# Optimization experiments

Measured on AMD Instinct MI355X. Metric: run time of the kernel, lower is better.

Reference implementation:

```python
import jax, jax.numpy as jnp
import numpy as np

DIM = 768
HEADS = 12
HEAD_DIM = DIM // HEADS
HIDDEN = 4 * DIM
LS_INIT = 1e-5
EPS = 1e-5


def layernorm(x, g, b):
    mu = jnp.mean(x, axis=-1, keepdims=True)
    var = jnp.mean(jnp.square(x - mu), axis=-1, keepdims=True)
    return (x - mu) * jax.lax.rsqrt(var + EPS) * g + b


def setup_inputs() -> dict:
    key = jax.random.key(0)
    ks = jax.random.split(key, 8)
    s = lambda fan_in: 1.0 / np.sqrt(fan_in)
    return {
        "x": jax.random.normal(ks[0], (8, 1024, DIM), dtype=jnp.float32),
        "ln1_g": jnp.ones((DIM,), jnp.float32),
        "ln1_b": jnp.zeros((DIM,), jnp.float32),
        "w_qkv": jax.random.uniform(ks[1], (3 * DIM, DIM), jnp.float32, -s(DIM), s(DIM)),
        "w_proj": jax.random.uniform(ks[2], (DIM, DIM), jnp.float32, -s(DIM), s(DIM)),
        "b_proj": jnp.zeros((DIM,), jnp.float32),
        "ls1_g": jnp.full((DIM,), LS_INIT, jnp.float32),
        "ln2_g": jnp.ones((DIM,), jnp.float32),
        "ln2_b": jnp.zeros((DIM,), jnp.float32),
        "w_fc1": jax.random.uniform(ks[3], (HIDDEN, DIM), jnp.float32, -s(DIM), s(DIM)),
        "b_fc1": jnp.zeros((HIDDEN,), jnp.float32),
        "w_fc2": jax.random.uniform(ks[4], (DIM, HIDDEN), jnp.float32, -s(HIDDEN), s(HIDDEN)),
        "b_fc2": jnp.zeros((DIM,), jnp.float32),
        "ls2_g": jnp.full((DIM,), LS_INIT, jnp.float32),
    }


def reference(x, ln1_g, ln1_b, w_qkv, w_proj, b_proj, ls1_g,
              ln2_g, ln2_b, w_fc1, b_fc1, w_fc2, b_fc2, ls2_g):
    B, N, C = x.shape
    # --- attention branch ---
    h = layernorm(x, ln1_g, ln1_b)
    qkv = h @ w_qkv.T  # [B,N,3C]
    qkv = qkv.reshape(B, N, 3, HEADS, HEAD_DIM)
    q, k, v = qkv[:, :, 0], qkv[:, :, 1], qkv[:, :, 2]  # [B,N,H,D]
    scale = 1.0 / np.sqrt(HEAD_DIM)
    attn = jnp.einsum("bqhd,bkhd->bhqk", q, k) * scale
    attn = jax.nn.softmax(attn, axis=-1)
    o = jnp.einsum("bhqk,bkhd->bqhd", attn, v).reshape(B, N, C)
    o = o @ w_proj.T + b_proj
    x = x + ls1_g * o
    # --- MLP branch ---
    h = layernorm(x, ln2_g, ln2_b)
    h = jax.nn.gelu(h @ w_fc1.T + b_fc1, approximate=False)
    h = h @ w_fc2.T + b_fc2
    x = x + ls2_g * h
    return x
```

## Files before the change

### kernel.cpp

```cpp
#include <hip/hip_runtime.h>
#include <cstdint>
#include <cstddef>

typedef __bf16 bf16x8 __attribute__((ext_vector_type(8)));
typedef __bf16 bf16x4 __attribute__((ext_vector_type(4)));
typedef float f32x4 __attribute__((ext_vector_type(4)));
typedef int i32x4 __attribute__((ext_vector_type(4)));
typedef int i32x8 __attribute__((ext_vector_type(8)));

__device__ __forceinline__ void gload16(const void* g, void* l) {
  __builtin_amdgcn_global_load_lds((const __attribute__((address_space(1))) void*)g,
                                   (__attribute__((address_space(3))) void*)l, 16, 0, 0);
}

__device__ __forceinline__ float exp2_fast(float x) {
  float r;
  asm("v_exp_f32 %0, %1" : "=v"(r) : "v"(x));
  return r;
}
__device__ __forceinline__ float rcp_fast(float x) {
  float r;
  asm("v_rcp_f32 %0, %1" : "=v"(r) : "v"(x));
  return r;
}

__device__ __forceinline__ unsigned char f32_to_fp8(float x) {
  int p = __builtin_amdgcn_cvt_pk_fp8_f32(x, 0.f, 0, false);
  return (unsigned char)(p & 0xff);
}
__device__ __forceinline__ unsigned int f32x4_to_fp8x4(float a, float b, float c, float d) {
  int p0 = __builtin_amdgcn_cvt_pk_fp8_f32(a, b, 0, false);
  int p1 = __builtin_amdgcn_cvt_pk_fp8_f32(c, d, 0, false);
  return (unsigned int)((p0 & 0xffff) | ((p1 & 0xffff) << 16));
}

template<int N> __device__ __forceinline__ void wait_vm() {
  if constexpr (N == 0) asm volatile("s_waitcnt vmcnt(0)" ::: "memory");
  else if constexpr (N == 4) asm volatile("s_waitcnt vmcnt(4)" ::: "memory");
  else if constexpr (N == 6) asm volatile("s_waitcnt vmcnt(6)" ::: "memory");
}

#define S_BARRIER() __builtin_amdgcn_s_barrier()
#define WAIT_VM4()  asm volatile("s_waitcnt vmcnt(4)" ::: "memory")
#define WAIT_VM0()  asm volatile("s_waitcnt vmcnt(0)" ::: "memory")
#define WAIT_LGKM() asm volatile("s_waitcnt lgkmcnt(0)" ::: "memory")

__global__ __launch_bounds__(256) void ln_kernel(const float* __restrict__ x,
    const float* __restrict__ g, const float* __restrict__ b,
    unsigned char* __restrict__ out)
{
  __shared__ float red[8];
  const int row = blockIdx.x, t = threadIdx.x;
  const float* xr = x + (size_t)row * 768;
  float v0 = xr[t], v1 = xr[t + 256], v2 = xr[t + 512];
  float s = v0 + v1 + v2;
  float q = v0 * v0 + v1 * v1 + v2 * v2;
  #pragma unroll
  for (int off = 32; off > 0; off >>= 1) {
    s += __shfl_xor(s, off, 64);
    q += __shfl_xor(q, off, 64);
  }
  const int w = t >> 6;
  if ((t & 63) == 0) { red[w] = s; red[4 + w] = q; }
  __syncthreads();
  s = red[0] + red[1] + red[2] + red[3];
  q = red[4] + red[5] + red[6] + red[7];
  const float mu = s * (1.0f / 768.0f);
  const float var = q * (1.0f / 768.0f) - mu * mu;
  const float rstd = rsqrtf(var + 1e-5f);
  unsigned char* orow = out + (size_t)row * 768;
  orow[t]       = f32_to_fp8((v0 - mu) * rstd * g[t]       + b[t]);
  orow[t + 256] = f32_to_fp8((v1 - mu) * rstd * g[t + 256] + b[t + 256]);
  orow[t + 512] = f32_to_fp8((v2 - mu) * rstd * g[t + 512] + b[t + 512]);
}

__global__ __launch_bounds__(256) void cast4_kernel(
    const float* __restrict__ i0, const float* __restrict__ i1,
    const float* __restrict__ i2, const float* __restrict__ i3,
    unsigned char* __restrict__ o0, unsigned char* __restrict__ o1,
    unsigned char* __restrict__ o2, unsigned char* __restrict__ o3)
{
  const int n0 = 2304 * 768 / 4, n1 = 768 * 768 / 4;
  const int n2 = 3072 * 768 / 4, n3 = 768 * 3072 / 4;
  const int total = n0 + n1 + n2 + n3;
  for (int i = blockIdx.x * 256 + threadIdx.x; i < total; i += gridDim.x * 256) {
    const float* in; unsigned char* out; int j = i;
    if (j < n0) { in = i0; out = o0; }
    else if ((j -= n0) < n1) { in = i1; out = o1; }
    else if ((j -= n1) < n2) { in = i2; out = o2; }
    else { j -= n2; in = i3; out = o3; }
    float4 v = ((const float4*)in)[j];
    ((unsigned int*)out)[j] = f32x4_to_fp8x4(v.x, v.y, v.z, v.w);
  }
}

template<int MODE>
__global__ __launch_bounds__(256) void gemm_kernel(
    const unsigned char* __restrict__ A, const unsigned char* __restrict__ W, int K,
    const float* __restrict__ bias, const float* __restrict__ resid,
    const float* __restrict__ ls, float* __restrict__ outf,
    unsigned char* __restrict__ outb,
    __bf16* __restrict__ qo, __bf16* __restrict__ ko, __bf16* __restrict__ vo)
{
  constexpr int BM = 128, BN = 64, BK = 128;
  constexpr int FM = 4, FN = 2;
  __shared__ unsigned char As[2 * BM * BK];
  __shared__ unsigned char Bs[2 * BN * BK];

  const int nx = gridDim.x;
  const int nwg = nx * gridDim.y;
  const int orig = blockIdx.x + nx * blockIdx.y;
  const int nid = (orig & 7) * (nwg >> 3) + (orig >> 3);
  const int bx = nid % nx, by = nid / nx;

  const int t = threadIdx.x;
  const int lane = t & 63;
  const int w = t >> 6;
  const int wm = w >> 1, wn = w & 1;
  const int m0 = by * BM, n0 = bx * BN;
  const int rl = lane & 15, gs = lane >> 4;

  f32x4 acc[FM][FN];
  #pragma unroll
  for (int i = 0; i < FM; ++i)
    #pragma unroll
    for (int j = 0; j < FN; ++j) acc[i][j] = { 0.f, 0.f, 0.f, 0.f };

  const unsigned char* Asrc[4];
  const unsigned char* Bsrc[2];
  #pragma unroll
  for (int i = 0; i < 4; ++i) {
    const int g = i * 256 + t, row = g >> 3, gc = g & 7;
    Asrc[i] = A + (size_t)(m0 + row) * K + ((gc ^ (row & 7)) << 4);
  }
  #pragma unroll
  for (int i = 0; i < 2; ++i) {
    const int g = i * 256 + t, row = g >> 3, gc = g & 7;
    Bsrc[i] = W + (size_t)(n0 + row) * K + ((gc ^ (row & 7)) << 4);
  }

  auto stage = [&](int kt, int buf) {
    const int k0 = kt << 7;
    #pragma unroll
    for (int i = 0; i < 4; ++i)
      gload16(Asrc[i] + k0, As + buf * 16384 + (i * 256 + t) * 16);
    #pragma unroll
    for (int i = 0; i < 2; ++i)
      gload16(Bsrc[i] + k0, Bs + buf * 8192 + (i * 256 + t) * 16);
  };

  auto ld32 = [&](const unsigned char* rowbase, int sw) -> i32x8 {
    const i32x4 lo = *(const i32x4*)(rowbase + (((2 * gs + 0) ^ sw) << 4));
    const i32x4 hi = *(const i32x4*)(rowbase + (((2 * gs + 1) ^ sw) << 4));
    i32x8 r;
    r[0] = lo[0]; r[1] = lo[1]; r[2] = lo[2]; r[3] = lo[3];
    r[4] = hi[0]; r[5] = hi[1]; r[6] = hi[2]; r[7] = hi[3];
    return r;
  };

  const int nk = K >> 7;
  stage(0, 0);

  #pragma unroll 2
  for (int kt = 0; kt < nk; ++kt) {
    const int cur = kt & 1;
    if (kt + 1 < nk) { stage(kt + 1, cur ^ 1); wait_vm<6>(); }
    else             { wait_vm<0>(); }
    S_BARRIER();

    const unsigned char* Ac = As + cur * 16384;
    const unsigned char* Bc = Bs + cur * 8192;
    i32x8 af[FM], bfr[FN];
    #pragma unroll
    for (int fm = 0; fm < FM; ++fm) {
      const int row = wm * 64 + fm * 16 + rl;
      af[fm] = ld32(Ac + row * 128, row & 7);
    }
    #pragma unroll
    for (int fn = 0; fn < FN; ++fn) {
      const int row = wn * 32 + fn * 16 + rl;
      bfr[fn] = ld32(Bc + row * 128, row & 7);
    }
    #pragma unroll
    for (int fm = 0; fm < FM; ++fm)
      #pragma unroll
      for (int fn = 0; fn < FN; ++fn)
        acc[fm][fn] = __builtin_amdgcn_mfma_scale_f32_16x16x128_f8f6f4(
            af[fm], bfr[fn], acc[fm][fn],
            0, 0,
            0, 0x7F7F7F7F,
            0, 0x7F7F7F7F);

    S_BARRIER();
  }

  #pragma unroll
  for (int fm = 0; fm < FM; ++fm) {
    const int rbase = m0 + wm * 64 + fm * 16 + gs * 4;
    #pragma unroll
    for (int fn = 0; fn < FN; ++fn) {
      const int c = n0 + wn * 32 + fn * 16 + rl;
      #pragma unroll
      for (int b = 0; b < 4; ++b) {
        const int r = rbase + b;
        const float val = acc[fm][fn][b];
        if constexpr (MODE == 0) {
          const int sec = c / 768;
          const int cc = c - sec * 768;
          const int hh = cc >> 6, d = cc & 63;
          const int batch = r >> 10, n = r & 1023;
          const size_t bh = (size_t)(batch * 12 + hh);
          if (sec == 0)      qo[(bh * 1024 + n) * 64 + d] = (__bf16)(val * 0.1803368801111204f);
          else if (sec == 1) ko[(bh * 1024 + n) * 64 + d] = (__bf16)val;
          else               vo[(bh * 64 + d) * 1024 + n] = (__bf16)val;
        } else if constexpr (MODE == 1) {
          const size_t idx = (size_t)r * 768 + c;
          outf[idx] = resid[idx] + ls[c] * (val + bias[c]);
        } else if constexpr (MODE == 2) {
          const float h = val + bias[c];
          const float z = h * (1.0f + 0.044715f * h * h);
          const float e = exp2_fast(2.3021181f * z);
          const float gl = h - h * rcp_fast(1.0f + e);
          outb[(size_t)r * 3072 + c] = f32_to_fp8(gl);
        } else {
          const size_t idx = (size_t)r * 768 + c;
          outf[idx] = resid[idx] + ls[c] * (val + bias[c]);
        }
      }
    }
  }
}

__global__ __launch_bounds__(256, 3) void attn_kernel(
    const __bf16* __restrict__ Q, const __bf16* __restrict__ Kb,
    const __bf16* __restrict__ Vt, unsigned char* __restrict__ Ob)
{
  __shared__ __bf16 Ks[2][64 * 64];
  __shared__ __bf16 Vs[2][64 * 64];
  __shared__ __bf16 P_lds[4][32 * 72];

  const int nid = blockIdx.x;
  const int b7 = nid & 7, rest = nid >> 3;
  const int qt = rest & 7;
  const int bh = b7 + ((rest >> 3) << 3);

  const int t = threadIdx.x, lane = t & 63, w = t >> 6;
  const int rl = lane & 15, gs = lane >> 4;
  const int q0 = qt * 128 + w * 32;
  const __bf16* Qh = Q  + (size_t)bh * 1024 * 64;
  const char*   Kg = (const char*)(Kb + (size_t)bh * 1024 * 64);
  const char*   Vg = (const char*)(Vt + (size_t)bh * 64 * 1024);
  __bf16* Pw = &P_lds[w][0];

  const int g0 = w * 64 + lane;
  const int g1 = 256 + g0;
  const int r0 = g0 >> 3, sb0 = (g0 & 7) ^ (r0 & 7);
  const int r1 = g1 >> 3, sb1 = (g1 & 7) ^ (r1 & 7);

  bf16x8 aq[2][2];
  #pragma unroll
  for (int m = 0; m < 2; ++m)
    #pragma unroll
    for (int ks = 0; ks < 2; ++ks)
      aq[m][ks] = *(const bf16x8*)(Qh + (size_t)(q0 + m * 16 + rl) * 64 + ks * 32 + gs * 8);

  f32x4 accO[2][4];
  #pragma unroll
  for (int m = 0; m < 2; ++m)
    #pragma unroll
    for (int d = 0; d < 4; ++d) accO[m][d] = { 0.f, 0.f, 0.f, 0.f };
  float L[2][4];
  #pragma unroll
  for (int m = 0; m < 2; ++m)
    #pragma unroll
    for (int b = 0; b < 4; ++b) L[m][b] = 0.f;

  {
    gload16(Kg + (size_t)r0 * 128 + sb0 * 16, (char*)Ks[0] + g0 * 16);
    gload16(Kg + (size_t)r1 * 128 + sb1 * 16, (char*)Ks[0] + g1 * 16);
    gload16(Vg + (size_t)r0 * 2048 + sb0 * 16, (char*)Vs[0] + g0 * 16);
    gload16(Vg + (size_t)r1 * 2048 + sb1 * 16, (char*)Vs[0] + g1 * 16);
  }

  for (int tile = 0; tile < 16; ++tile) {
    const int cur = tile & 1;
    if (tile + 1 < 16) {
      const int nxt = cur ^ 1;
      const size_t kofs = (size_t)(tile + 1) * 64;
      gload16(Kg + (kofs + r0) * 128 + sb0 * 16, (char*)Ks[nxt] + g0 * 16);
      gload16(Kg + (kofs + r1) * 128 + sb1 * 16, (char*)Ks[nxt] + g1 * 16);
      gload16(Vg + (size_t)r0 * 2048 + kofs * 2 + sb0 * 16, (char*)Vs[nxt] + g0 * 16);
      gload16(Vg + (size_t)r1 * 2048 + kofs * 2 + sb1 * 16, (char*)Vs[nxt] + g1 * 16);
      WAIT_VM4();
    } else {
      WAIT_VM0();
    }
    S_BARRIER();

    const __bf16* Kc = Ks[cur];
    const __bf16* Vc = Vs[cur];

    f32x4 s[2][4];
    #pragma unroll
    for (int m = 0; m < 2; ++m)
      #pragma unroll
      for (int ct = 0; ct < 4; ++ct) s[m][ct] = { 0.f, 0.f, 0.f, 0.f };
    __builtin_amdgcn_s_setprio(1);
    #pragma unroll
    for (int ct = 0; ct < 4; ++ct) {
      #pragma unroll
      for (int ks = 0; ks < 2; ++ks) {
        const int row = ct * 16 + rl;
        const int blk = (ks * 4 + gs) ^ (row & 7);
        bf16x8 kf = *(const bf16x8*)(Kc + row * 64 + blk * 8);
        s[0][ct] = __builtin_amdgcn_mfma_f32_16x16x32_bf16(aq[0][ks], kf, s[0][ct], 0, 0, 0);
        s[1][ct] = __builtin_amdgcn_mfma_f32_16x16x32_bf16(aq[1][ks], kf, s[1][ct], 0, 0, 0);
      }
    }
    __builtin_amdgcn_s_setprio(0);

    #pragma unroll
    for (int m = 0; m < 2; ++m) {
      #pragma unroll
      for (int b = 0; b < 4; ++b) {
        float rs = 0.f;
        #pragma unroll
        for (int ct = 0; ct < 4; ++ct) {
          const float p = exp2_fast(s[m][ct][b]);
          rs += p;
          Pw[(m * 16 + gs * 4 + b) * 72 + ct * 16 + rl] = (__bf16)p;
        }
        L[m][b] += rs;
      }
    }

    WAIT_LGKM();
    bf16x8 ap[2][2];
    #pragma unroll
    for (int m = 0; m < 2; ++m)
      #pragma unroll
      for (int ks = 0; ks < 2; ++ks)
        ap[m][ks] = *(const bf16x8*)(Pw + (m * 16 + rl) * 72 + ks * 32 + gs * 8);

    __builtin_amdgcn_s_setprio(1);
    #pragma unroll
    for (int dt = 0; dt < 4; ++dt) {
      #pragma unroll
      for (int ks = 0; ks < 2; ++ks) {
        const int row = dt * 16 + rl;
        const int blk = (ks * 4 + gs) ^ (row & 7);
        bf16x8 vf = *(const bf16x8*)(Vc + row * 64 + blk * 8);
        accO[0][dt] = __builtin_amdgcn_mfma_f32_16x16x32_bf16(ap[0][ks], vf, accO[0][dt], 0, 0, 0);
        accO[1][dt] = __builtin_amdgcn_mfma_f32_16x16x32_bf16(ap[1][ks], vf, accO[1][dt], 0, 0, 0);
      }
    }
    __builtin_amdgcn_s_setprio(0);

    S_BARRIER();
  }

  float invL[2][4];
  #pragma unroll
  for (int m = 0; m < 2; ++m)
    #pragma unroll
    for (int b = 0; b < 4; ++b) {
      float rs = L[m][b];
      #pragma unroll
      for (int off = 1; off < 16; off <<= 1) rs += __shfl_xor(rs, off, 16);
      invL[m][b] = 1.0f / rs;
    }

  const int batch = bh / 12, hh = bh - batch * 12;
  #pragma unroll
  for (int m = 0; m < 2; ++m) {
    const size_t rowbase = (size_t)batch * 1024 + qt * 128 + w * 32 + m * 16 + gs * 4;
    #pragma unroll
    for (int dt = 0; dt < 4; ++dt)
      #pragma unroll
      for (int b = 0; b < 4; ++b)
        Ob[(rowbase + b) * 768 + hh * 64 + dt * 16 + rl] = f32_to_fp8(accO[m][dt][b] * invL[m][b]);
  }
}

extern "C" void kernel_launch(void* const* d_in, const int* in_sizes, int n_in,
                              void* d_out, int out_size, void* d_ws, size_t ws_size,
                              hipStream_t stream) {
  const float* x      = (const float*)d_in[0];
  const float* ln1_g  = (const float*)d_in[1];
  const float* ln1_b  = (const float*)d_in[2];
  const float* w_qkv  = (const float*)d_in[3];
  const float* w_proj = (const float*)d_in[4];
  const float* b_proj = (const float*)d_in[5];
  const float* ls1    = (const float*)d_in[6];
  const float* ln2_g  = (const float*)d_in[7];
  const float* ln2_b  = (const float*)d_in[8];
  const float* w_fc1  = (const float*)d_in[9];
  const float* b_fc1  = (const float*)d_in[10];
  const float* w_fc2  = (const float*)d_in[11];
  const float* b_fc2  = (const float*)d_in[12];
  const float* ls2    = (const float*)d_in[13];
  float* out = (float*)d_out;

  char* ws = (char*)d_ws;
  size_t off = 0;
  auto alloc = [&](size_t bytes) { char* p = ws + off; off += (bytes + 255) & ~(size_t)255; return p; };
  unsigned char* h1    = (unsigned char*)alloc(8192ull * 768);
  unsigned char* wqkv8 = (unsigned char*)alloc(2304ull * 768);
  unsigned char* wprj8 = (unsigned char*)alloc(768ull * 768);
  unsigned char* wfc18 = (unsigned char*)alloc(3072ull * 768);
  unsigned char* wfc28 = (unsigned char*)alloc(768ull * 3072);
  __bf16* Qb    = (__bf16*)alloc(8192ull * 768 * 2);
  __bf16* Kb    = (__bf16*)alloc(8192ull * 768 * 2);
  __bf16* Vt    = (__bf16*)alloc(8192ull * 768 * 2);
  float*  out1  = (float*)alloc(8192ull * 768 * 4);
  unsigned char* fc1o = (unsigned char*)alloc(8192ull * 3072);
  unsigned char* h2   = (unsigned char*)alloc(8192ull * 768);

  ln_kernel<<<8192, 256, 0, stream>>>(x, ln1_g, ln1_b, h1);
  cast4_kernel<<<2048, 256, 0, stream>>>(w_qkv, w_proj, w_fc1, w_fc2,
                                         wqkv8, wprj8, wfc18, wfc28);

  gemm_kernel<0><<<dim3(36, 64), 256, 0, stream>>>(h1, wqkv8, 768,
      nullptr, nullptr, nullptr, nullptr, nullptr, Qb, Kb, Vt);

  attn_kernel<<<96 * 8, 256, 0, stream>>>(Qb, Kb, Vt, h1);

  gemm_kernel<1><<<dim3(12, 64), 256, 0, stream>>>(h1, wprj8, 768,
      b_proj, x, ls1, out1, nullptr, nullptr, nullptr, nullptr);

  ln_kernel<<<8192, 256, 0, stream>>>(out1, ln2_g, ln2_b, h2);

  gemm_kernel<2><<<dim3(48, 64), 256, 0, stream>>>(h2, wfc18, 768,
      b_fc1, nullptr, nullptr, nullptr, fc1o, nullptr, nullptr, nullptr);

  gemm_kernel<3><<<dim3(12, 64), 256, 0, stream>>>(fc1o, wfc28, 3072,
      b_fc2, out1, ls2, out, nullptr, nullptr, nullptr, nullptr);
}
```

Baseline: 182.8 us.

## Load V tiles directly from global into registers instead of staging through LDS

The attention kernel no longer double-buffers V through shared memory. Each wave now reads its V fragments straight from global memory into registers for each key tile, issuing those loads before the softmax so their latency can overlap it. This halves the kernel's LDS footprint and raises the launch-bounds occupancy hint from 3 to 4 blocks per CU. The trade-off is that all four waves fetch the same V tile redundantly through the cache, with extra register pressure and less latency hiding than the async LDS prefetch gave.

```diff
diff --git a/kernel.cpp b/kernel.cpp
--- a/kernel.cpp
+++ b/kernel.cpp
@@ -36,13 +36,12 @@
 
 template<int N> __device__ __forceinline__ void wait_vm() {
   if constexpr (N == 0) asm volatile("s_waitcnt vmcnt(0)" ::: "memory");
+  else if constexpr (N == 2) asm volatile("s_waitcnt vmcnt(2)" ::: "memory");
   else if constexpr (N == 4) asm volatile("s_waitcnt vmcnt(4)" ::: "memory");
   else if constexpr (N == 6) asm volatile("s_waitcnt vmcnt(6)" ::: "memory");
 }
 
 #define S_BARRIER() __builtin_amdgcn_s_barrier()
-#define WAIT_VM4()  asm volatile("s_waitcnt vmcnt(4)" ::: "memory")
-#define WAIT_VM0()  asm volatile("s_waitcnt vmcnt(0)" ::: "memory")
 #define WAIT_LGKM() asm volatile("s_waitcnt lgkmcnt(0)" ::: "memory")
 
 __global__ __launch_bounds__(256) void ln_kernel(const float* __restrict__ x,
@@ -231,12 +230,11 @@
   }
 }
 
-__global__ __launch_bounds__(256, 3) void attn_kernel(
+__global__ __launch_bounds__(256, 4) void attn_kernel(
     const __bf16* __restrict__ Q, const __bf16* __restrict__ Kb,
     const __bf16* __restrict__ Vt, unsigned char* __restrict__ Ob)
 {
   __shared__ __bf16 Ks[2][64 * 64];
-  __shared__ __bf16 Vs[2][64 * 64];
   __shared__ __bf16 P_lds[4][32 * 72];
 
   const int nid = blockIdx.x;
@@ -249,7 +247,7 @@
   const int q0 = qt * 128 + w * 32;
   const __bf16* Qh = Q  + (size_t)bh * 1024 * 64;
   const char*   Kg = (const char*)(Kb + (size_t)bh * 1024 * 64);
-  const char*   Vg = (const char*)(Vt + (size_t)bh * 64 * 1024);
+  const __bf16* Vh = Vt + (size_t)bh * 64 * 1024;
   __bf16* Pw = &P_lds[w][0];
 
   const int g0 = w * 64 + lane;
@@ -275,30 +273,22 @@
     #pragma unroll
     for (int b = 0; b < 4; ++b) L[m][b] = 0.f;
 
-  {
-    gload16(Kg + (size_t)r0 * 128 + sb0 * 16, (char*)Ks[0] + g0 * 16);
-    gload16(Kg + (size_t)r1 * 128 + sb1 * 16, (char*)Ks[0] + g1 * 16);
-    gload16(Vg + (size_t)r0 * 2048 + sb0 * 16, (char*)Vs[0] + g0 * 16);
-    gload16(Vg + (size_t)r1 * 2048 + sb1 * 16, (char*)Vs[0] + g1 * 16);
-  }
+  gload16(Kg + (size_t)r0 * 128 + sb0 * 16, (char*)Ks[0] + g0 * 16);
+  gload16(Kg + (size_t)r1 * 128 + sb1 * 16, (char*)Ks[0] + g1 * 16);
 
   for (int tile = 0; tile < 16; ++tile) {
     const int cur = tile & 1;
     if (tile + 1 < 16) {
-      const int nxt = cur ^ 1;
       const size_t kofs = (size_t)(tile + 1) * 64;
-      gload16(Kg + (kofs + r0) * 128 + sb0 * 16, (char*)Ks[nxt] + g0 * 16);
-      gload16(Kg + (kofs + r1) * 128 + sb1 * 16, (char*)Ks[nxt] + g1 * 16);
-      gload16(Vg + (size_t)r0 * 2048 + kofs * 2 + sb0 * 16, (char*)Vs[nxt] + g0 * 16);
-      gload16(Vg + (size_t)r1 * 2048 + kofs * 2 + sb1 * 16, (char*)Vs[nxt] + g1 * 16);
-      WAIT_VM4();
+      gload16(Kg + (kofs + r0) * 128 + sb0 * 16, (char*)Ks[cur ^ 1] + g0 * 16);
+      gload16(Kg + (kofs + r1) * 128 + sb1 * 16, (char*)Ks[cur ^ 1] + g1 * 16);
+      wait_vm<2>();
     } else {
-      WAIT_VM0();
+      wait_vm<0>();
     }
     S_BARRIER();
 
     const __bf16* Kc = Ks[cur];
-    const __bf16* Vc = Vs[cur];
 
     f32x4 s[2][4];
     #pragma unroll
@@ -318,6 +308,14 @@
       }
     }
     __builtin_amdgcn_s_setprio(0);
+
+    bf16x8 vf[4][2];
+    #pragma unroll
+    for (int dt = 0; dt < 4; ++dt)
+      #pragma unroll
+      for (int ks = 0; ks < 2; ++ks)
+        vf[dt][ks] = *(const bf16x8*)(Vh + (size_t)(dt * 16 + rl) * 1024
+                                      + tile * 64 + ks * 32 + gs * 8);
 
     #pragma unroll
     for (int m = 0; m < 2; ++m) {
@@ -347,11 +345,8 @@
     for (int dt = 0; dt < 4; ++dt) {
       #pragma unroll
       for (int ks = 0; ks < 2; ++ks) {
-        const int row = dt * 16 + rl;
-        const int blk = (ks * 4 + gs) ^ (row & 7);
-        bf16x8 vf = *(const bf16x8*)(Vc + row * 64 + blk * 8);
-        accO[0][dt] = __builtin_amdgcn_mfma_f32_16x16x32_bf16(ap[0][ks], vf, accO[0][dt], 0, 0, 0);
-        accO[1][dt] = __builtin_amdgcn_mfma_f32_16x16x32_bf16(ap[1][ks], vf, accO[1][dt], 0, 0, 0);
+        accO[0][dt] = __builtin_amdgcn_mfma_f32_16x16x32_bf16(ap[0][ks], vf[dt][ks], accO[0][dt], 0, 0, 0);
+        accO[1][dt] = __builtin_amdgcn_mfma_f32_16x16x32_bf16(ap[1][ks], vf[dt][ks], accO[1][dt], 0, 0, 0);
       }
     }
     __builtin_amdgcn_s_setprio(0);
```

Result: slower. 210.5 us (+15.1%).
